# Performance work log

Hardware: AMD Instinct MI355X
Metric: run time of the kernel (lower is better)

## Reference

```python
import jax, jax.numpy as jnp
import numpy as np

B, S, HID = 2, 2048, 2048
H, KVH, D = 32, 4, 128
EPS = 1e-6
ROPE_THETA = 1e6
INIT = 0.02


def setup_inputs() -> dict:
    key = jax.random.key(0)
    ks = jax.random.split(key, 6)
    hidden_states = jax.random.normal(ks[0], (B, S, HID), jnp.float32)
    q_w = jax.random.normal(ks[1], (HID, H * D), jnp.float32) * INIT
    k_w = jax.random.normal(ks[2], (HID, KVH * D), jnp.float32) * INIT
    v_w = jax.random.normal(ks[3], (HID, KVH * D), jnp.float32) * INIT
    o_w = jax.random.normal(ks[4], (H * D, HID), jnp.float32) * INIT
    q_norm_w = jnp.ones((D,), jnp.float32)
    k_norm_w = jnp.ones((D,), jnp.float32)
    # rotary embeddings, computed once per position (B, S, D)
    pos = jnp.arange(S, dtype=jnp.float32)
    inv_freq = 1.0 / (ROPE_THETA ** (jnp.arange(0, D, 2, dtype=jnp.float32) / D))
    freqs = pos[:, None] * inv_freq[None, :]          # (S, D/2)
    emb = jnp.concatenate([freqs, freqs], axis=-1)    # (S, D)
    cos = jnp.broadcast_to(jnp.cos(emb)[None], (B, S, D))
    sin = jnp.broadcast_to(jnp.sin(emb)[None], (B, S, D))
    # causal mask (is_causal=True, sliding_window=None)
    attn_mask = jnp.tril(jnp.ones((S, S), bool))[None, None]  # (1,1,S,S)
    return {"hidden_states": hidden_states, "cos": cos, "sin": sin,
            "q_w": q_w, "k_w": k_w, "v_w": v_w, "o_w": o_w,
            "q_norm_w": q_norm_w, "k_norm_w": k_norm_w, "attn_mask": attn_mask}


def _rms_norm(x, w):
    xf = x.astype(jnp.float32)
    var = jnp.mean(jax.lax.square(xf), axis=-1, keepdims=True)
    return (w * (xf * jax.lax.rsqrt(var + EPS))).astype(x.dtype)


def _rotate_half(x):
    x1, x2 = jnp.split(x, 2, axis=-1)
    return jnp.concatenate([-x2, x1], axis=-1)


def _apply_rope(q, k, cos, sin):
    # q: (B,H,S,D), k: (B,KVH,S,D); cos/sin: (B,S,D) -> (B,1,S,D)
    cos = cos[:, None]
    sin = sin[:, None]
    q = q * cos + _rotate_half(q) * sin
    k = k * cos + _rotate_half(k) * sin
    return q, k


def reference(hidden_states, cos, sin, q_w, k_w, v_w, o_w, q_norm_w, k_norm_w, attn_mask):
    b, s, _ = hidden_states.shape
    scaling = D ** (-0.5)
    # projections + per-head QK RMSNorm
    q = _rms_norm((hidden_states @ q_w).reshape(b, s, H, D), q_norm_w)
    k = _rms_norm((hidden_states @ k_w).reshape(b, s, KVH, D), k_norm_w)
    v = (hidden_states @ v_w).reshape(b, s, KVH, D)
    q = jnp.transpose(q, (0, 2, 1, 3))   # (b,H,s,D)
    k = jnp.transpose(k, (0, 2, 1, 3))   # (b,KVH,s,D)
    v = jnp.transpose(v, (0, 2, 1, 3))
    q, k = _apply_rope(q, k, cos, sin)
    # GQA: repeat KV heads across groups
    groups = H // KVH
    k = jnp.repeat(k, groups, axis=1)    # (b,H,s,D)
    v = jnp.repeat(v, groups, axis=1)
    # eager softmax attention (fp32 softmax)
    scores = jnp.einsum('bhqd,bhkd->bhqk', q, k).astype(jnp.float32) * scaling
    scores = jnp.where(attn_mask, scores, jnp.float32(-1e30))
    probs = jax.nn.softmax(scores, axis=-1).astype(q.dtype)
    attn = jnp.einsum('bhqk,bhkd->bhqd', probs, v)
    attn = jnp.transpose(attn, (0, 2, 1, 3)).reshape(b, s, H * D)
    return attn @ o_w
```

## Files before the change

kernel.cpp:

```cpp
#include <hip/hip_runtime.h>
#include <hip/hip_bf16.h>

typedef unsigned short u16;
typedef __attribute__((ext_vector_type(4))) float f32x4;
typedef __attribute__((ext_vector_type(16))) float f32x16;
typedef __attribute__((ext_vector_type(8))) short bf16x8;
typedef __attribute__((ext_vector_type(4))) unsigned u32x4;

#define B_ 2
#define S_ 2048
#define HID_ 2048
#define H_ 32
#define KVH_ 4
#define D_ 128
#define M_ 4096
#define NQ_ 4096
#define NKV_ 512

typedef const __attribute__((address_space(1))) void gconst_void;
typedef __attribute__((address_space(3))) void lds_void;

static __device__ __forceinline__ void gload_lds16(const void* g, void* l) {
  __builtin_amdgcn_global_load_lds((gconst_void*)g, (lds_void*)l, 16, 0, 0);
}

#define WAITV(N) asm volatile("s_waitcnt vmcnt(" #N ")" ::: "memory")
#define WAITL0() asm volatile("s_waitcnt lgkmcnt(0)" ::: "memory")

static __device__ __forceinline__ u16 f2b(float f) {
  union { float f; unsigned i; } x; x.f = f;
  return (u16)((x.i + 0x7fffu + ((x.i >> 16) & 1u)) >> 16);
}
static __device__ __forceinline__ float b2f(u16 u) {
  union { unsigned i; float f; } x; x.i = ((unsigned)u) << 16;
  return x.f;
}

__global__ void k_cvt(const float* __restrict__ in, u16* __restrict__ out, int n4) {
  int i = blockIdx.x * blockDim.x + threadIdx.x;
  int stride = gridDim.x * blockDim.x;
  for (; i < n4; i += stride) {
    float4 v = reinterpret_cast<const float4*>(in)[i];
    ushort4 o;
    o.x = f2b(v.x); o.y = f2b(v.y); o.z = f2b(v.z); o.w = f2b(v.w);
    reinterpret_cast<ushort4*>(out)[i] = o;
  }
}

__global__ __launch_bounds__(256) void k_transpose(const float* __restrict__ W,
                                                   u16* __restrict__ Wt, int K, int N) {
  __shared__ u16 t[64][72];
  int n0 = blockIdx.x * 64, k0 = blockIdx.y * 64;
  int tid = threadIdx.x;
  int r = tid >> 4;
  int c4 = (tid & 15) * 4;
#pragma unroll
  for (int i = 0; i < 4; i++) {
    int k = r + i * 16;
    float4 v = *reinterpret_cast<const float4*>(W + (size_t)(k0 + k) * N + n0 + c4);
    t[k][c4 + 0] = f2b(v.x); t[k][c4 + 1] = f2b(v.y);
    t[k][c4 + 2] = f2b(v.z); t[k][c4 + 3] = f2b(v.w);
  }
  __syncthreads();
#pragma unroll
  for (int i = 0; i < 4; i++) {
    int n = r + i * 16;
    ushort4 o;
    o.x = t[c4 + 0][n]; o.y = t[c4 + 1][n]; o.z = t[c4 + 2][n]; o.w = t[c4 + 3][n];
    *reinterpret_cast<ushort4*>(Wt + (size_t)(n0 + n) * K + k0 + c4) = o;
  }
}

__device__ __forceinline__ void gemm_core(const u16* __restrict__ A, const u16* __restrict__ Bt,
                                          int K, int m0, int n0,
                                          u16* As, u16* Bs, f32x4 (&acc)[4][4]) {
  const int tid = threadIdx.x;
  const int lane = tid & 63;
  const int wid = tid >> 6;
  const int wr = wid >> 1, wc = wid & 1;
  const int lrow = lane & 15;
  const int hi = lane >> 4;
  const f32x4 zz = {0.f, 0.f, 0.f, 0.f};
#pragma unroll
  for (int i = 0; i < 4; i++)
#pragma unroll
    for (int j = 0; j < 4; j++) acc[i][j] = zz;

  const int srow = tid >> 3;
  const int sc16 = tid & 7;
  const int nk = K >> 6;
  int cur = 0;

#pragma unroll
  for (int rep = 0; rep < 4; rep++) {
    int row = rep * 32 + srow;
    int gcol = ((sc16 ^ (row & 7)) << 3);
    gload_lds16(A + (size_t)(m0 + row) * K + gcol, As + row * 64 + sc16 * 8);
    gload_lds16(Bt + (size_t)(n0 + row) * K + gcol, Bs + row * 64 + sc16 * 8);
  }
  __syncthreads();

  for (int t = 0; t < nk; t++) {
    if (t + 1 < nk) {
      int nxt = cur ^ 1;
      int kb = (t + 1) << 6;
#pragma unroll
      for (int rep = 0; rep < 4; rep++) {
        int row = rep * 32 + srow;
        int gcol = kb + ((sc16 ^ (row & 7)) << 3);
        gload_lds16(A + (size_t)(m0 + row) * K + gcol, As + nxt * 8192 + row * 64 + sc16 * 8);
        gload_lds16(Bt + (size_t)(n0 + row) * K + gcol, Bs + nxt * 8192 + row * 64 + sc16 * 8);
      }
    }
    const u16* Ac = As + cur * 8192;
    const u16* Bc = Bs + cur * 8192;
#pragma unroll
    for (int kc = 0; kc < 2; kc++) {
      bf16x8 af[4], bfr[4];
#pragma unroll
      for (int i = 0; i < 4; i++) {
        int row = wr * 64 + i * 16 + lrow;
        af[i] = *reinterpret_cast<const bf16x8*>(Ac + row * 64 + ((((kc << 2) + hi) ^ (row & 7)) << 3));
      }
#pragma unroll
      for (int j = 0; j < 4; j++) {
        int row = wc * 64 + j * 16 + lrow;
        bfr[j] = *reinterpret_cast<const bf16x8*>(Bc + row * 64 + ((((kc << 2) + hi) ^ (row & 7)) << 3));
      }
#pragma unroll
      for (int i = 0; i < 4; i++)
#pragma unroll
        for (int j = 0; j < 4; j++)
          acc[i][j] = __builtin_amdgcn_mfma_f32_16x16x32_bf16(af[i], bfr[j], acc[i][j], 0, 0, 0);
    }
    __syncthreads();
    cur ^= 1;
  }
}

__global__ __launch_bounds__(512, 2) void k_gemm_q8(const u16* __restrict__ A,
    const u16* __restrict__ Bt, u16* __restrict__ qb) {
  __shared__ u16 Ash[2][2][128 * 64];
  __shared__ u16 Bsh[2][2][128 * 64];
  const int bid = blockIdx.x;
  const int wg = (bid & 7) * 32 + (bid >> 3);
  const int mt = wg & 15, nt = wg >> 4;
  const int m0 = mt * 256, n0 = nt * 256;
  const int K = HID_, nk = K >> 6;
  const int tid = threadIdx.x, lane = tid & 63;
  const int wv = tid >> 6, wr = wv >> 2, wc = wv & 3;
  const int lrow = lane & 15, hi4 = lane >> 4;

  const int s0r = tid >> 3, sc = tid & 7;
  const int s1r = (tid + 512) >> 3;

  auto stgA = [&](int h, int t, int d) {
    gload_lds16(A + (size_t)(m0 + h * 128 + s0r) * K + t * 64 + ((sc ^ (s0r & 7)) << 3),
                &Ash[d][h][s0r * 64 + sc * 8]);
    gload_lds16(A + (size_t)(m0 + h * 128 + s1r) * K + t * 64 + ((sc ^ (s1r & 7)) << 3),
                &Ash[d][h][s1r * 64 + sc * 8]);
  };
  auto stgB = [&](int h, int t, int d) {
    gload_lds16(Bt + (size_t)(n0 + h * 128 + s0r) * K + t * 64 + ((sc ^ (s0r & 7)) << 3),
                &Bsh[d][h][s0r * 64 + sc * 8]);
    gload_lds16(Bt + (size_t)(n0 + h * 128 + s1r) * K + t * 64 + ((sc ^ (s1r & 7)) << 3),
                &Bsh[d][h][s1r * 64 + sc * 8]);
  };

  f32x4 acc[8][4];
  const f32x4 zz = {0.f, 0.f, 0.f, 0.f};
#pragma unroll
  for (int f = 0; f < 8; f++)
#pragma unroll
    for (int j = 0; j < 4; j++) acc[f][j] = zz;

  bf16x8 af[4][2], bfr[2][2];

  auto lda = [&](int mh, int d) {
#pragma unroll
    for (int fi = 0; fi < 4; fi++) {
      int row = fi * 32 + wr * 16 + lrow;
#pragma unroll
      for (int kk = 0; kk < 2; kk++)
        af[fi][kk] = *reinterpret_cast<const bf16x8*>(
            &Ash[d][mh][row * 64 + ((((kk << 2) + hi4) ^ (row & 7)) << 3)]);
    }
  };
  auto ldb = [&](int nh, int d) {
#pragma unroll
    for (int ji = 0; ji < 2; ji++) {
      int row = ji * 64 + wc * 16 + lrow;
#pragma unroll
      for (int kk = 0; kk < 2; kk++)
        bfr[ji][kk] = *reinterpret_cast<const bf16x8*>(
            &Bsh[d][nh][row * 64 + ((((kk << 2) + hi4) ^ (row & 7)) << 3)]);
    }
  };
  auto mq = [&](int mh, int nh) {
    __builtin_amdgcn_s_setprio(1);
#pragma unroll
    for (int kk = 0; kk < 2; kk++)
#pragma unroll
      for (int fi = 0; fi < 4; fi++)
#pragma unroll
        for (int ji = 0; ji < 2; ji++)
          acc[mh * 4 + fi][nh * 2 + ji] = __builtin_amdgcn_mfma_f32_16x16x32_bf16(
              af[fi][kk], bfr[ji][kk], acc[mh * 4 + fi][nh * 2 + ji], 0, 0, 0);
    __builtin_amdgcn_s_setprio(0);
  };

  stgA(0, 0, 0); stgB(0, 0, 0); stgA(1, 0, 0); stgB(1, 0, 0);
  WAITV(0);
  __builtin_amdgcn_s_barrier();

  for (int t = 0; t < nk; t++) {
    const int d = t & 1, nd = d ^ 1;
    const bool pre = (t + 1 < nk);
    if (pre) { stgA(0, t + 1, nd); stgB(0, t + 1, nd); }
    lda(0, d); ldb(0, d);
    WAITV(6);
    __builtin_amdgcn_sched_barrier(0);
    __builtin_amdgcn_s_barrier();
    WAITL0();
    __builtin_amdgcn_sched_barrier(0);
    mq(0, 0);
    __builtin_amdgcn_s_barrier();
    if (pre) stgA(1, t + 1, nd);
    lda(1, d);
    WAITV(6);
    __builtin_amdgcn_sched_barrier(0);
    __builtin_amdgcn_s_barrier();
    WAITL0();
    __builtin_amdgcn_sched_barrier(0);
    mq(1, 0);
    __builtin_amdgcn_s_barrier();
    if (pre) stgB(1, t + 1, nd);
    ldb(1, d);
    __builtin_amdgcn_sched_barrier(0);
    __builtin_amdgcn_s_barrier();
    WAITL0();
    __builtin_amdgcn_sched_barrier(0);
    mq(1, 1);
    __builtin_amdgcn_s_barrier();
    lda(0, d);
    WAITV(4);
    __builtin_amdgcn_sched_barrier(0);
    __builtin_amdgcn_s_barrier();
    WAITL0();
    __builtin_amdgcn_sched_barrier(0);
    mq(0, 1);
    __builtin_amdgcn_s_barrier();
  }

  const int lr4 = hi4 * 4, lc = lane & 15;
#pragma unroll
  for (int f = 0; f < 8; f++)
#pragma unroll
    for (int j = 0; j < 4; j++)
#pragma unroll
      for (int rr = 0; rr < 4; rr++) {
        int m = m0 + f * 32 + wr * 16 + lr4 + rr;
        int ncol = n0 + j * 64 + wc * 16 + lc;
        int b = m >> 11, s = m & (S_ - 1);
        int head = ncol >> 7, dd = ncol & 127;
        qb[(((size_t)b * H_ + head) * S_ + s) * D_ + dd] = f2b(acc[f][j][rr]);
      }
}

__global__ __launch_bounds__(256, 2) void k_gemm_kv(const u16* __restrict__ hb,
    const u16* __restrict__ kwt, const u16* __restrict__ vwt,
    u16* __restrict__ kb, u16* __restrict__ vb) {
  __shared__ u16 As[2 * 128 * 64], Bs[2 * 128 * 64];
  const int bid = blockIdx.x;
  const int wg = (bid & 7) * 32 + (bid >> 3);
  const int mt = wg & 31, nt = wg >> 5;
  const bool isv = nt >= 4;
  const int head = isv ? nt - 4 : nt;
  const u16* Bt = isv ? vwt : kwt;
  f32x4 acc[4][4];
  gemm_core(hb, Bt, HID_, mt * 128, head * 128, As, Bs, acc);
  const int lane = threadIdx.x & 63;
  const int wid = threadIdx.x >> 6;
  const int wr = wid >> 1, wc = wid & 1;
  const int lr4 = (lane >> 4) * 4, lc = lane & 15;
#pragma unroll
  for (int i = 0; i < 4; i++)
#pragma unroll
    for (int j = 0; j < 4; j++)
#pragma unroll
      for (int r = 0; r < 4; r++) {
        int m = mt * 128 + wr * 64 + i * 16 + lr4 + r;
        int d = wc * 64 + j * 16 + lc;
        int b = m >> 11, s = m & (S_ - 1);
        u16 val = f2b(acc[i][j][r]);
        if (isv) vb[(((size_t)b * KVH_ + head) * D_ + d) * S_ + s] = val;
        else     kb[(((size_t)b * KVH_ + head) * S_ + s) * D_ + d] = val;
      }
}

__global__ __launch_bounds__(256, 2) void k_gemm_o(const u16* __restrict__ ab,
    const u16* __restrict__ owt, float* __restrict__ out) {
  __shared__ u16 As[2 * 128 * 64], Bs[2 * 128 * 64];
  const int bid = blockIdx.x;
  const int wg = (bid & 7) * 64 + (bid >> 3);
  const int mt = wg & 31, nt = wg >> 5;
  f32x4 acc[4][4];
  gemm_core(ab, owt, NQ_, mt * 128, nt * 128, As, Bs, acc);
  const int lane = threadIdx.x & 63;
  const int wid = threadIdx.x >> 6;
  const int wr = wid >> 1, wc = wid & 1;
  const int lr4 = (lane >> 4) * 4, lc = lane & 15;
#pragma unroll
  for (int i = 0; i < 4; i++)
#pragma unroll
    for (int j = 0; j < 4; j++)
#pragma unroll
      for (int r = 0; r < 4; r++) {
        int m = mt * 128 + wr * 64 + i * 16 + lr4 + r;
        int n = nt * 128 + wc * 64 + j * 16 + lc;
        out[(size_t)m * HID_ + n] = acc[i][j][r];
      }
}

__global__ __launch_bounds__(256) void k_norm_rope(u16* __restrict__ qb, u16* __restrict__ kb,
    const float* __restrict__ cosp, const float* __restrict__ sinp,
    const float* __restrict__ qnw, const float* __restrict__ knw) {
  int row = blockIdx.x * 4 + (threadIdx.x >> 6);
  int lane = threadIdx.x & 63;
  const int QROWS = B_ * H_ * S_;
  u16* ptr; const float* nw; int b, s;
  if (row < QROWS) {
    ptr = qb + (size_t)row * D_; nw = qnw;
    s = row & (S_ - 1); b = row / (H_ * S_);
  } else {
    int r2 = row - QROWS;
    ptr = kb + (size_t)r2 * D_; nw = knw;
    s = r2 & (S_ - 1); b = r2 / (KVH_ * S_);
  }
  int d = lane * 2;
  float x0 = b2f(ptr[d]), x1 = b2f(ptr[d + 1]);
  float ss = x0 * x0 + x1 * x1;
#pragma unroll
  for (int m = 1; m < 64; m <<= 1) ss += __shfl_xor(ss, m);
  float inv = rsqrtf(ss * (1.0f / 128.0f) + 1e-6f);
  x0 = x0 * inv * nw[d]; x1 = x1 * inv * nw[d + 1];
  float p0 = __shfl_xor(x0, 32), p1 = __shfl_xor(x1, 32);
  float r0 = (lane < 32) ? -p0 : p0;
  float r1 = (lane < 32) ? -p1 : p1;
  const float* cp = cosp + ((size_t)b * S_ + s) * D_;
  const float* sp = sinp + ((size_t)b * S_ + s) * D_;
  ptr[d]     = f2b(x0 * cp[d]     + r0 * sp[d]);
  ptr[d + 1] = f2b(x1 * cp[d + 1] + r1 * sp[d + 1]);
}

__global__ __launch_bounds__(512, 2) void k_attn(const u16* __restrict__ q,
    const u16* __restrict__ k, const u16* __restrict__ vt, u16* __restrict__ out) {
  __shared__ u16 Kb[2 * 64 * 128];
  __shared__ u16 Vb[2 * 128 * 64];
  const int bid = blockIdx.x;
  const int wg = (bid & 7) * 32 + (bid >> 3);
  const int qx = wg & 3, bh = wg >> 2;
  const int b = bh >> 5, h = bh & 31;
  const int kvh = h >> 3;
  const int tid = threadIdx.x, lane = tid & 63, w = tid >> 6;
  const int lq = lane & 31, hi = lane >> 5;
  const u16* qp  = q  + ((size_t)(b * H_ + h) * S_) * D_;
  const u16* kp  = k  + ((size_t)(b * KVH_ + kvh) * S_) * D_;
  const u16* vtp = vt + ((size_t)(b * KVH_ + kvh) * D_) * S_;

  const int rowKa = tid >> 4;
  const int colK  = ((tid & 15) ^ (rowKa & 15)) << 3;
  const int rowVa = tid >> 3;
  const int colV  = ((tid & 7) ^ (rowVa & 7)) << 3;

  const float KSC = 0.08838834764831845f * 1.44269504088896340f;
  const f32x16 z16 = {0.f};

  int cur = 0;
  for (int half = 0; half < 2; half++) {
    const int qt = half ? (7 - qx) : qx;
    const int q0 = qt * 256;
    const int last = 4 * qt + 3;
    const int qg = q0 + 32 * w + lq;

    {
      u16* kd = Kb + cur * 8192 + tid * 8;
      u16* vd = Vb + cur * 8192 + tid * 8;
      gload_lds16(kp + (size_t)rowKa * D_ + colK, kd);
      gload_lds16(kp + (size_t)(rowKa + 32) * D_ + colK, kd + 4096);
      gload_lds16(vtp + (size_t)rowVa * S_ + colV, vd);
      gload_lds16(vtp + (size_t)(rowVa + 64) * S_ + colV, vd + 4096);
    }

    bf16x8 qf[8];
#pragma unroll
    for (int ds = 0; ds < 8; ds++)
      qf[ds] = *reinterpret_cast<const bf16x8*>(qp + (size_t)qg * D_ + ds * 16 + hi * 8);

    f32x16 oacc[4];
#pragma unroll
    for (int dt = 0; dt < 4; dt++) oacc[dt] = z16;
    float mrun = -1e30f, lrun = 0.f;

    __syncthreads();

    for (int nt = 0; nt <= last; nt++) {
      const int n0 = nt * 64;
      if (nt < last) {
        const int n1 = n0 + 64;
        u16* kd = Kb + (cur ^ 1) * 8192 + tid * 8;
        u16* vd = Vb + (cur ^ 1) * 8192 + tid * 8;
        gload_lds16(kp + (size_t)(n1 + rowKa) * D_ + colK, kd);
        gload_lds16(kp + (size_t)(n1 + rowKa + 32) * D_ + colK, kd + 4096);
        gload_lds16(vtp + (size_t)rowVa * S_ + n1 + colV, vd);
        gload_lds16(vtp + (size_t)(rowVa + 64) * S_ + n1 + colV, vd + 4096);
      }
      const u16* Kc = Kb + cur * 8192;
      const u16* Vc = Vb + cur * 8192;

      const bool skip = (n0 > q0 + 32 * w + 31);
      if (!skip) {
        const bool needmask = (n0 + 63 > q0 + 32 * w);

        f32x16 sacc[2];
        sacc[0] = z16; sacc[1] = z16;
#pragma unroll
        for (int ds = 0; ds < 8; ds++) {
          const int sl = (((ds << 1) + hi) ^ (lq & 15)) << 3;
          bf16x8 ka0 = *reinterpret_cast<const bf16x8*>(Kc + lq * 128 + sl);
          bf16x8 ka1 = *reinterpret_cast<const bf16x8*>(Kc + (lq + 32) * 128 + sl);
          __builtin_amdgcn_s_setprio(1);
          sacc[0] = __builtin_amdgcn_mfma_f32_32x32x16_bf16(ka0, qf[ds], sacc[0], 0, 0, 0);
          sacc[1] = __builtin_amdgcn_mfma_f32_32x32x16_bf16(ka1, qf[ds], sacc[1], 0, 0, 0);
          __builtin_amdgcn_s_setprio(0);
        }

        float tm = -1e30f;
#pragma unroll
        for (int t = 0; t < 2; t++)
#pragma unroll
          for (int r = 0; r < 16; r++) {
            float s2 = sacc[t][r] * KSC;
            if (needmask) {
              int kvg = n0 + 32 * t + (r & 3) + 8 * (r >> 2) + 4 * hi;
              if (kvg > qg) s2 = -1e30f;
            }
            sacc[t][r] = s2;
            tm = fmaxf(tm, s2);
          }
        tm = fmaxf(tm, __shfl_xor(tm, 32));
        if (__any(tm > mrun + 8.f)) {
          float mn = fmaxf(mrun, tm);
          float al = exp2f(mrun - mn);
          mrun = mn;
          lrun *= al;
#pragma unroll
          for (int r = 0; r < 16; r++) {
            float ar = __shfl(al, (r & 3) + 8 * (r >> 2) + 4 * hi);
#pragma unroll
            for (int dt = 0; dt < 4; dt++) oacc[dt][r] *= ar;
          }
        }
        float rs = 0.f;
#pragma unroll
        for (int t = 0; t < 2; t++)
#pragma unroll
          for (int r = 0; r < 16; r++) {
            float pv = exp2f(sacc[t][r] - mrun);
            sacc[t][r] = pv;
            rs += pv;
          }
        rs += __shfl_xor(rs, 32);
        lrun += rs;

        u32x4 pa[4];
#pragma unroll
        for (int t = 0; t < 2; t++)
#pragma unroll
          for (int ksl = 0; ksl < 2; ksl++) {
            unsigned wa, wb, wc2, wd;
            asm("v_cvt_pk_bf16_f32 %0, %1, %2" : "=v"(wa)
                : "v"(sacc[t][8 * ksl + 0]), "v"(sacc[t][8 * ksl + 1]));
            asm("v_cvt_pk_bf16_f32 %0, %1, %2" : "=v"(wb)
                : "v"(sacc[t][8 * ksl + 2]), "v"(sacc[t][8 * ksl + 3]));
            asm("v_cvt_pk_bf16_f32 %0, %1, %2" : "=v"(wc2)
                : "v"(sacc[t][8 * ksl + 4]), "v"(sacc[t][8 * ksl + 5]));
            asm("v_cvt_pk_bf16_f32 %0, %1, %2" : "=v"(wd)
                : "v"(sacc[t][8 * ksl + 6]), "v"(sacc[t][8 * ksl + 7]));
            asm("v_permlane32_swap_b32 %0, %1" : "+v"(wa), "+v"(wc2));
            asm("v_permlane32_swap_b32 %0, %1" : "+v"(wb), "+v"(wd));
            u32x4 t4 = {wa, wb, wc2, wd};
            pa[t * 2 + ksl] = t4;
          }

#pragma unroll
        for (int ks = 0; ks < 4; ks++) {
          bf16x8 paf = __builtin_bit_cast(bf16x8, pa[ks]);
          bf16x8 bv[4];
#pragma unroll
          for (int dt = 0; dt < 4; dt++) {
            int rowv = dt * 32 + lq;
            bv[dt] = *reinterpret_cast<const bf16x8*>(
                Vc + rowv * 64 + ((((ks << 1) + hi) ^ (rowv & 7)) << 3));
          }
          __builtin_amdgcn_s_setprio(1);
#pragma unroll
          for (int dt = 0; dt < 4; dt++)
            oacc[dt] = __builtin_amdgcn_mfma_f32_32x32x16_bf16(paf, bv[dt], oacc[dt], 0, 0, 0);
          __builtin_amdgcn_s_setprio(0);
        }
      }
      __syncthreads();
      cur ^= 1;
    }

    float linv = 1.0f / lrun;
#pragma unroll
    for (int r = 0; r < 16; r++) {
      const int idx_r = (r & 3) + 8 * (r >> 2) + 4 * hi;
      float lr = __shfl(linv, idx_r);
      size_t base = ((size_t)b * S_ + (q0 + 32 * w + idx_r)) * NQ_ + h * D_ + lq;
#pragma unroll
      for (int dt = 0; dt < 4; dt++)
        out[base + dt * 32] = f2b(oacc[dt][r] * lr);
    }
  }
}

extern "C" void kernel_launch(void* const* d_in, const int* in_sizes, int n_in,
                              void* d_out, int out_size, void* d_ws, size_t ws_size,
                              hipStream_t stream) {
  const float* hidden = (const float*)d_in[0];
  const float* cosp   = (const float*)d_in[1];
  const float* sinp   = (const float*)d_in[2];
  const float* q_w    = (const float*)d_in[3];
  const float* k_w    = (const float*)d_in[4];
  const float* v_w    = (const float*)d_in[5];
  const float* o_w    = (const float*)d_in[6];
  const float* qnw    = (const float*)d_in[7];
  const float* knw    = (const float*)d_in[8];

  char* p = (char*)d_ws;
  u16* hb  = (u16*)p; p += (size_t)M_ * HID_ * 2;
  u16* qwt = (u16*)p; p += (size_t)NQ_ * HID_ * 2;
  u16* kwt = (u16*)p; p += (size_t)NKV_ * HID_ * 2;
  u16* vwt = (u16*)p; p += (size_t)NKV_ * HID_ * 2;
  u16* owt = (u16*)p; p += (size_t)HID_ * NQ_ * 2;
  u16* qb  = (u16*)p; p += (size_t)B_ * H_ * S_ * D_ * 2;
  u16* kb  = (u16*)p; p += (size_t)B_ * KVH_ * S_ * D_ * 2;
  u16* vb  = (u16*)p; p += (size_t)B_ * KVH_ * S_ * D_ * 2;
  u16* ab  = (u16*)p; p += (size_t)M_ * NQ_ * 2;

  k_cvt<<<2048, 256, 0, stream>>>(hidden, hb, M_ * HID_ / 4);
  k_transpose<<<dim3(NQ_ / 64, HID_ / 64), 256, 0, stream>>>(q_w, qwt, HID_, NQ_);
  k_transpose<<<dim3(NKV_ / 64, HID_ / 64), 256, 0, stream>>>(k_w, kwt, HID_, NKV_);
  k_transpose<<<dim3(NKV_ / 64, HID_ / 64), 256, 0, stream>>>(v_w, vwt, HID_, NKV_);
  k_transpose<<<dim3(HID_ / 64, NQ_ / 64), 256, 0, stream>>>(o_w, owt, NQ_, HID_);
  k_gemm_q8<<<256, 512, 0, stream>>>(hb, qwt, qb);
  k_gemm_kv<<<256, 256, 0, stream>>>(hb, kwt, vwt, kb, vb);
  k_norm_rope<<<(B_ * H_ * S_ + B_ * KVH_ * S_) / 4, 256, 0, stream>>>(qb, kb, cosp, sinp, qnw, knw);
  k_attn<<<256, 512, 0, stream>>>(qb, kb, vb, ab);
  k_gemm_o<<<512, 256, 0, stream>>>(ab, owt, (float*)d_out);
}
```

Baseline: 361.2 us.

## Fuse prep kernels, fold softmax scale into norm, split attention grid, repipeline Q GEMM

```diff
diff --git a/kernel.cpp b/kernel.cpp
--- a/kernel.cpp
+++ b/kernel.cpp
@@ -26,6 +26,8 @@
 
 #define WAITV(N) asm volatile("s_waitcnt vmcnt(" #N ")" ::: "memory")
 #define WAITL0() asm volatile("s_waitcnt lgkmcnt(0)" ::: "memory")
+#define SBAR() __builtin_amdgcn_s_barrier()
+#define SCHED0() __builtin_amdgcn_sched_barrier(0)
 
 static __device__ __forceinline__ u16 f2b(float f) {
   union { float f; unsigned i; } x; x.f = f;
@@ -35,22 +37,14 @@
   union { unsigned i; float f; } x; x.i = ((unsigned)u) << 16;
   return x.f;
 }
-
-__global__ void k_cvt(const float* __restrict__ in, u16* __restrict__ out, int n4) {
-  int i = blockIdx.x * blockDim.x + threadIdx.x;
-  int stride = gridDim.x * blockDim.x;
-  for (; i < n4; i += stride) {
-    float4 v = reinterpret_cast<const float4*>(in)[i];
-    ushort4 o;
-    o.x = f2b(v.x); o.y = f2b(v.y); o.z = f2b(v.z); o.w = f2b(v.w);
-    reinterpret_cast<ushort4*>(out)[i] = o;
-  }
-}
-
-__global__ __launch_bounds__(256) void k_transpose(const float* __restrict__ W,
-                                                   u16* __restrict__ Wt, int K, int N) {
-  __shared__ u16 t[64][72];
-  int n0 = blockIdx.x * 64, k0 = blockIdx.y * 64;
+static __device__ __forceinline__ float max3f(float a, float b, float c) {
+  float d;
+  asm("v_max3_f32 %0, %1, %2, %3" : "=v"(d) : "v"(a), "v"(b), "v"(c));
+  return d;
+}
+
+static __device__ __forceinline__ void tr_tile(const float* __restrict__ W,
+    u16* __restrict__ Wt, int K, int N, int n0, int k0, u16 (*t)[72]) {
   int tid = threadIdx.x;
   int r = tid >> 4;
   int c4 = (tid & 15) * 4;
@@ -68,6 +62,38 @@
     ushort4 o;
     o.x = t[c4 + 0][n]; o.y = t[c4 + 1][n]; o.z = t[c4 + 2][n]; o.w = t[c4 + 3][n];
     *reinterpret_cast<ushort4*>(Wt + (size_t)(n0 + n) * K + k0 + c4) = o;
+  }
+}
+
+__global__ __launch_bounds__(256) void k_prep(const float* __restrict__ hidden, u16* __restrict__ hb,
+    const float* __restrict__ qw, u16* __restrict__ qwt,
+    const float* __restrict__ kw, u16* __restrict__ kwt,
+    const float* __restrict__ vw, u16* __restrict__ vwt,
+    const float* __restrict__ ow, u16* __restrict__ owt) {
+  __shared__ u16 t[64][72];
+  const int bid = blockIdx.x;
+  if (bid < 2048) {
+    const int n4 = M_ * HID_ / 4;
+    int i = bid * 256 + threadIdx.x;
+    const int stride = 2048 * 256;
+    for (; i < n4; i += stride) {
+      float4 v = reinterpret_cast<const float4*>(hidden)[i];
+      ushort4 o;
+      o.x = f2b(v.x); o.y = f2b(v.y); o.z = f2b(v.z); o.w = f2b(v.w);
+      reinterpret_cast<ushort4*>(hb)[i] = o;
+    }
+  } else if (bid < 4096) {
+    int l = bid - 2048;
+    tr_tile(qw, qwt, HID_, NQ_, (l & 63) * 64, (l >> 6) * 64, t);
+  } else if (bid < 4352) {
+    int l = bid - 4096;
+    tr_tile(kw, kwt, HID_, NKV_, (l & 7) * 64, (l >> 3) * 64, t);
+  } else if (bid < 4608) {
+    int l = bid - 4352;
+    tr_tile(vw, vwt, HID_, NKV_, (l & 7) * 64, (l >> 3) * 64, t);
+  } else {
+    int l = bid - 4608;
+    tr_tile(ow, owt, NQ_, HID_, (l & 31) * 64, (l >> 5) * 64, t);
   }
 }
 
@@ -174,15 +200,15 @@
 #pragma unroll
     for (int j = 0; j < 4; j++) acc[f][j] = zz;
 
-  bf16x8 af[4][2], bfr[2][2];
-
-  auto lda = [&](int mh, int d) {
+  bf16x8 af0[4][2], af1[4][2], bfr[2][2];
+
+  auto lda = [&](bf16x8 (&dst)[4][2], int mh, int d) {
 #pragma unroll
     for (int fi = 0; fi < 4; fi++) {
       int row = fi * 32 + wr * 16 + lrow;
 #pragma unroll
       for (int kk = 0; kk < 2; kk++)
-        af[fi][kk] = *reinterpret_cast<const bf16x8*>(
+        dst[fi][kk] = *reinterpret_cast<const bf16x8*>(
             &Ash[d][mh][row * 64 + ((((kk << 2) + hi4) ^ (row & 7)) << 3)]);
     }
   };
@@ -196,7 +222,7 @@
             &Bsh[d][nh][row * 64 + ((((kk << 2) + hi4) ^ (row & 7)) << 3)]);
     }
   };
-  auto mq = [&](int mh, int nh) {
+  auto mq = [&](bf16x8 (&afh)[4][2], int mh, int nh) {
     __builtin_amdgcn_s_setprio(1);
 #pragma unroll
     for (int kk = 0; kk < 2; kk++)
@@ -205,51 +231,39 @@
 #pragma unroll
         for (int ji = 0; ji < 2; ji++)
           acc[mh * 4 + fi][nh * 2 + ji] = __builtin_amdgcn_mfma_f32_16x16x32_bf16(
-              af[fi][kk], bfr[ji][kk], acc[mh * 4 + fi][nh * 2 + ji], 0, 0, 0);
+              afh[fi][kk], bfr[ji][kk], acc[mh * 4 + fi][nh * 2 + ji], 0, 0, 0);
     __builtin_amdgcn_s_setprio(0);
   };
 
-  stgA(0, 0, 0); stgB(0, 0, 0); stgA(1, 0, 0); stgB(1, 0, 0);
-  WAITV(0);
-  __builtin_amdgcn_s_barrier();
+  stgA(0, 0, 0); stgA(1, 0, 0); stgB(0, 0, 0); stgB(1, 0, 0);
+  WAITV(2); SCHED0();
+  SBAR(); SCHED0();
 
   for (int t = 0; t < nk; t++) {
     const int d = t & 1, nd = d ^ 1;
     const bool pre = (t + 1 < nk);
-    if (pre) { stgA(0, t + 1, nd); stgB(0, t + 1, nd); }
-    lda(0, d); ldb(0, d);
-    WAITV(6);
-    __builtin_amdgcn_sched_barrier(0);
-    __builtin_amdgcn_s_barrier();
-    WAITL0();
-    __builtin_amdgcn_sched_barrier(0);
-    mq(0, 0);
-    __builtin_amdgcn_s_barrier();
+    lda(af0, 0, d); ldb(0, d);
+    if (pre) stgA(0, t + 1, nd);
+    SCHED0(); SBAR();
+    WAITL0(); SCHED0();
+    mq(af0, 0, 0);
+    SBAR(); SCHED0();
+    lda(af1, 1, d);
     if (pre) stgA(1, t + 1, nd);
-    lda(1, d);
-    WAITV(6);
-    __builtin_amdgcn_sched_barrier(0);
-    __builtin_amdgcn_s_barrier();
-    WAITL0();
-    __builtin_amdgcn_sched_barrier(0);
-    mq(1, 0);
-    __builtin_amdgcn_s_barrier();
+    WAITV(4); SCHED0(); SBAR();
+    WAITL0(); SCHED0();
+    mq(af1, 1, 0);
+    SBAR(); SCHED0();
+    ldb(1, d);
+    if (pre) stgB(0, t + 1, nd);
+    SCHED0(); SBAR();
+    WAITL0(); SCHED0();
+    mq(af1, 1, 1);
+    SBAR(); SCHED0();
     if (pre) stgB(1, t + 1, nd);
-    ldb(1, d);
-    __builtin_amdgcn_sched_barrier(0);
-    __builtin_amdgcn_s_barrier();
-    WAITL0();
-    __builtin_amdgcn_sched_barrier(0);
-    mq(1, 1);
-    __builtin_amdgcn_s_barrier();
-    lda(0, d);
-    WAITV(4);
-    __builtin_amdgcn_sched_barrier(0);
-    __builtin_amdgcn_s_barrier();
-    WAITL0();
-    __builtin_amdgcn_sched_barrier(0);
-    mq(0, 1);
-    __builtin_amdgcn_s_barrier();
+    WAITV(2); SCHED0(); SBAR();
+    mq(af0, 0, 1);
+    SBAR(); SCHED0();
   }
 
   const int lr4 = hi4 * 4, lc = lane & 15;
@@ -328,21 +342,23 @@
   int row = blockIdx.x * 4 + (threadIdx.x >> 6);
   int lane = threadIdx.x & 63;
   const int QROWS = B_ * H_ * S_;
-  u16* ptr; const float* nw; int b, s;
+  u16* ptr; const float* nw; int b, s; float os;
   if (row < QROWS) {
     ptr = qb + (size_t)row * D_; nw = qnw;
     s = row & (S_ - 1); b = row / (H_ * S_);
+    os = 0.08838834764831845f * 1.44269504088896340f;
   } else {
     int r2 = row - QROWS;
     ptr = kb + (size_t)r2 * D_; nw = knw;
     s = r2 & (S_ - 1); b = r2 / (KVH_ * S_);
+    os = 1.0f;
   }
   int d = lane * 2;
   float x0 = b2f(ptr[d]), x1 = b2f(ptr[d + 1]);
   float ss = x0 * x0 + x1 * x1;
 #pragma unroll
   for (int m = 1; m < 64; m <<= 1) ss += __shfl_xor(ss, m);
-  float inv = rsqrtf(ss * (1.0f / 128.0f) + 1e-6f);
+  float inv = rsqrtf(ss * (1.0f / 128.0f) + 1e-6f) * os;
   x0 = x0 * inv * nw[d]; x1 = x1 * inv * nw[d + 1];
   float p0 = __shfl_xor(x0, 32), p1 = __shfl_xor(x1, 32);
   float r0 = (lane < 32) ? -p0 : p0;
@@ -353,13 +369,13 @@
   ptr[d + 1] = f2b(x1 * cp[d + 1] + r1 * sp[d + 1]);
 }
 
-__global__ __launch_bounds__(512, 2) void k_attn(const u16* __restrict__ q,
+__global__ __launch_bounds__(512, 4) void k_attn(const u16* __restrict__ q,
     const u16* __restrict__ k, const u16* __restrict__ vt, u16* __restrict__ out) {
   __shared__ u16 Kb[2 * 64 * 128];
   __shared__ u16 Vb[2 * 128 * 64];
   const int bid = blockIdx.x;
-  const int wg = (bid & 7) * 32 + (bid >> 3);
-  const int qx = wg & 3, bh = wg >> 2;
+  const int qt = (bid < 256) ? (7 - (bid >> 6)) : ((bid - 256) >> 6);
+  const int bh = bid & 63;
   const int b = bh >> 5, h = bh & 31;
   const int kvh = h >> 3;
   const int tid = threadIdx.x, lane = tid & 63, w = tid >> 6;
@@ -373,157 +389,154 @@
   const int rowVa = tid >> 3;
   const int colV  = ((tid & 7) ^ (rowVa & 7)) << 3;
 
-  const float KSC = 0.08838834764831845f * 1.44269504088896340f;
   const f32x16 z16 = {0.f};
+  const int q0 = qt * 256;
+  const int last = 4 * qt + 3;
+  const int qg = q0 + 32 * w + lq;
+
+  {
+    u16* kd = Kb + tid * 8;
+    u16* vd = Vb + tid * 8;
+    gload_lds16(kp + (size_t)rowKa * D_ + colK, kd);
+    gload_lds16(kp + (size_t)(rowKa + 32) * D_ + colK, kd + 4096);
+    gload_lds16(vtp + (size_t)rowVa * S_ + colV, vd);
+    gload_lds16(vtp + (size_t)(rowVa + 64) * S_ + colV, vd + 4096);
+  }
+
+  bf16x8 qf[8];
+#pragma unroll
+  for (int ds = 0; ds < 8; ds++)
+    qf[ds] = *reinterpret_cast<const bf16x8*>(qp + (size_t)qg * D_ + ds * 16 + hi * 8);
+
+  f32x16 oacc[4];
+#pragma unroll
+  for (int dt = 0; dt < 4; dt++) oacc[dt] = z16;
+  float mrun = -1e30f, lrun = 0.f;
+
+  __syncthreads();
 
   int cur = 0;
-  for (int half = 0; half < 2; half++) {
-    const int qt = half ? (7 - qx) : qx;
-    const int q0 = qt * 256;
-    const int last = 4 * qt + 3;
-    const int qg = q0 + 32 * w + lq;
-
-    {
-      u16* kd = Kb + cur * 8192 + tid * 8;
-      u16* vd = Vb + cur * 8192 + tid * 8;
-      gload_lds16(kp + (size_t)rowKa * D_ + colK, kd);
-      gload_lds16(kp + (size_t)(rowKa + 32) * D_ + colK, kd + 4096);
-      gload_lds16(vtp + (size_t)rowVa * S_ + colV, vd);
-      gload_lds16(vtp + (size_t)(rowVa + 64) * S_ + colV, vd + 4096);
-    }
-
-    bf16x8 qf[8];
-#pragma unroll
-    for (int ds = 0; ds < 8; ds++)
-      qf[ds] = *reinterpret_cast<const bf16x8*>(qp + (size_t)qg * D_ + ds * 16 + hi * 8);
-
-    f32x16 oacc[4];
-#pragma unroll
-    for (int dt = 0; dt < 4; dt++) oacc[dt] = z16;
-    float mrun = -1e30f, lrun = 0.f;
-
+  for (int nt = 0; nt <= last; nt++) {
+    const int n0 = nt * 64;
+    if (nt < last) {
+      const int n1 = n0 + 64;
+      u16* kd = Kb + (cur ^ 1) * 8192 + tid * 8;
+      u16* vd = Vb + (cur ^ 1) * 8192 + tid * 8;
+      gload_lds16(kp + (size_t)(n1 + rowKa) * D_ + colK, kd);
+      gload_lds16(kp + (size_t)(n1 + rowKa + 32) * D_ + colK, kd + 4096);
+      gload_lds16(vtp + (size_t)rowVa * S_ + n1 + colV, vd);
+      gload_lds16(vtp + (size_t)(rowVa + 64) * S_ + n1 + colV, vd + 4096);
+    }
+    const u16* Kc = Kb + cur * 8192;
+    const u16* Vc = Vb + cur * 8192;
+
+    const bool skip = (n0 > q0 + 32 * w + 31);
+    if (!skip) {
+      const bool needmask = (n0 + 63 > q0 + 32 * w);
+
+      f32x16 sacc[2];
+      sacc[0] = z16; sacc[1] = z16;
+#pragma unroll
+      for (int ds = 0; ds < 8; ds++) {
+        const int sl = (((ds << 1) + hi) ^ (lq & 15)) << 3;
+        bf16x8 ka0 = *reinterpret_cast<const bf16x8*>(Kc + lq * 128 + sl);
+        bf16x8 ka1 = *reinterpret_cast<const bf16x8*>(Kc + (lq + 32) * 128 + sl);
+        __builtin_amdgcn_s_setprio(1);
+        sacc[0] = __builtin_amdgcn_mfma_f32_32x32x16_bf16(ka0, qf[ds], sacc[0], 0, 0, 0);
+        sacc[1] = __builtin_amdgcn_mfma_f32_32x32x16_bf16(ka1, qf[ds], sacc[1], 0, 0, 0);
+        __builtin_amdgcn_s_setprio(0);
+      }
+
+      if (needmask) {
+#pragma unroll
+        for (int t = 0; t < 2; t++)
+#pragma unroll
+          for (int r = 0; r < 16; r++) {
+            int kvg = n0 + 32 * t + (r & 3) + 8 * (r >> 2) + 4 * hi;
+            if (kvg > qg) sacc[t][r] = -1e30f;
+          }
+      }
+      float tm = fmaxf(sacc[0][0], sacc[0][1]);
+#pragma unroll
+      for (int i = 1; i < 16; i++) {
+        const int e0 = 2 * i, e1 = 2 * i + 1;
+        tm = max3f(tm, sacc[e0 >> 4][e0 & 15], sacc[e1 >> 4][e1 & 15]);
+      }
+      tm = fmaxf(tm, __shfl_xor(tm, 32));
+      if (__any(tm > mrun + 8.f)) {
+        float mn = fmaxf(mrun, tm);
+        float al = exp2f(mrun - mn);
+        mrun = mn;
+        lrun *= al;
+#pragma unroll
+        for (int r = 0; r < 16; r++) {
+          float ar = __shfl(al, (r & 3) + 8 * (r >> 2) + 4 * hi);
+#pragma unroll
+          for (int dt = 0; dt < 4; dt++) oacc[dt][r] *= ar;
+        }
+      }
+      float rs = 0.f;
+#pragma unroll
+      for (int t = 0; t < 2; t++)
+#pragma unroll
+        for (int r = 0; r < 16; r++) {
+          float pv = exp2f(sacc[t][r] - mrun);
+          sacc[t][r] = pv;
+          rs += pv;
+        }
+      rs += __shfl_xor(rs, 32);
+      lrun += rs;
+
+      u32x4 pa[4];
+#pragma unroll
+      for (int t = 0; t < 2; t++)
+#pragma unroll
+        for (int ksl = 0; ksl < 2; ksl++) {
+          unsigned wa, wb, wc2, wd;
+          asm("v_cvt_pk_bf16_f32 %0, %1, %2" : "=v"(wa)
+              : "v"(sacc[t][8 * ksl + 0]), "v"(sacc[t][8 * ksl + 1]));
+          asm("v_cvt_pk_bf16_f32 %0, %1, %2" : "=v"(wb)
+              : "v"(sacc[t][8 * ksl + 2]), "v"(sacc[t][8 * ksl + 3]));
+          asm("v_cvt_pk_bf16_f32 %0, %1, %2" : "=v"(wc2)
+              : "v"(sacc[t][8 * ksl + 4]), "v"(sacc[t][8 * ksl + 5]));
+          asm("v_cvt_pk_bf16_f32 %0, %1, %2" : "=v"(wd)
+              : "v"(sacc[t][8 * ksl + 6]), "v"(sacc[t][8 * ksl + 7]));
+          asm("v_permlane32_swap_b32 %0, %1" : "+v"(wa), "+v"(wc2));
+          asm("v_permlane32_swap_b32 %0, %1" : "+v"(wb), "+v"(wd));
+          u32x4 t4 = {wa, wb, wc2, wd};
+          pa[t * 2 + ksl] = t4;
+        }
+
+#pragma unroll
+      for (int ks = 0; ks < 4; ks++) {
+        bf16x8 paf = __builtin_bit_cast(bf16x8, pa[ks]);
+        bf16x8 bv[4];
+#pragma unroll
+        for (int dt = 0; dt < 4; dt++) {
+          int rowv = dt * 32 + lq;
+          bv[dt] = *reinterpret_cast<const bf16x8*>(
+              Vc + rowv * 64 + ((((ks << 1) + hi) ^ (rowv & 7)) << 3));
+        }
+        __builtin_amdgcn_s_setprio(1);
+#pragma unroll
+        for (int dt = 0; dt < 4; dt++)
+          oacc[dt] = __builtin_amdgcn_mfma_f32_32x32x16_bf16(paf, bv[dt], oacc[dt], 0, 0, 0);
+        __builtin_amdgcn_s_setprio(0);
+      }
+    }
     __syncthreads();
-
-    for (int nt = 0; nt <= last; nt++) {
-      const int n0 = nt * 64;
-      if (nt < last) {
-        const int n1 = n0 + 64;
-        u16* kd = Kb + (cur ^ 1) * 8192 + tid * 8;
-        u16* vd = Vb + (cur ^ 1) * 8192 + tid * 8;
-        gload_lds16(kp + (size_t)(n1 + rowKa) * D_ + colK, kd);
-        gload_lds16(kp + (size_t)(n1 + rowKa + 32) * D_ + colK, kd + 4096);
-        gload_lds16(vtp + (size_t)rowVa * S_ + n1 + colV, vd);
-        gload_lds16(vtp + (size_t)(rowVa + 64) * S_ + n1 + colV, vd + 4096);
-      }
-      const u16* Kc = Kb + cur * 8192;
-      const u16* Vc = Vb + cur * 8192;
-
-      const bool skip = (n0 > q0 + 32 * w + 31);
-      if (!skip) {
-        const bool needmask = (n0 + 63 > q0 + 32 * w);
-
-        f32x16 sacc[2];
-        sacc[0] = z16; sacc[1] = z16;
-#pragma unroll
-        for (int ds = 0; ds < 8; ds++) {
-          const int sl = (((ds << 1) + hi) ^ (lq & 15)) << 3;
-          bf16x8 ka0 = *reinterpret_cast<const bf16x8*>(Kc + lq * 128 + sl);
-          bf16x8 ka1 = *reinterpret_cast<const bf16x8*>(Kc + (lq + 32) * 128 + sl);
-          __builtin_amdgcn_s_setprio(1);
-          sacc[0] = __builtin_amdgcn_mfma_f32_32x32x16_bf16(ka0, qf[ds], sacc[0], 0, 0, 0);
-          sacc[1] = __builtin_amdgcn_mfma_f32_32x32x16_bf16(ka1, qf[ds], sacc[1], 0, 0, 0);
-          __builtin_amdgcn_s_setprio(0);
-        }
-
-        float tm = -1e30f;
-#pragma unroll
-        for (int t = 0; t < 2; t++)
-#pragma unroll
-          for (int r = 0; r < 16; r++) {
-            float s2 = sacc[t][r] * KSC;
-            if (needmask) {
-              int kvg = n0 + 32 * t + (r & 3) + 8 * (r >> 2) + 4 * hi;
-              if (kvg > qg) s2 = -1e30f;
-            }
-            sacc[t][r] = s2;
-            tm = fmaxf(tm, s2);
-          }
-        tm = fmaxf(tm, __shfl_xor(tm, 32));
-        if (__any(tm > mrun + 8.f)) {
-          float mn = fmaxf(mrun, tm);
-          float al = exp2f(mrun - mn);
-          mrun = mn;
-          lrun *= al;
-#pragma unroll
-          for (int r = 0; r < 16; r++) {
-            float ar = __shfl(al, (r & 3) + 8 * (r >> 2) + 4 * hi);
-#pragma unroll
-            for (int dt = 0; dt < 4; dt++) oacc[dt][r] *= ar;
-          }
-        }
-        float rs = 0.f;
-#pragma unroll
-        for (int t = 0; t < 2; t++)
-#pragma unroll
-          for (int r = 0; r < 16; r++) {
-            float pv = exp2f(sacc[t][r] - mrun);
-            sacc[t][r] = pv;
-            rs += pv;
-          }
-        rs += __shfl_xor(rs, 32);
-        lrun += rs;
-
-        u32x4 pa[4];
-#pragma unroll
-        for (int t = 0; t < 2; t++)
-#pragma unroll
-          for (int ksl = 0; ksl < 2; ksl++) {
-            unsigned wa, wb, wc2, wd;
-            asm("v_cvt_pk_bf16_f32 %0, %1, %2" : "=v"(wa)
-                : "v"(sacc[t][8 * ksl + 0]), "v"(sacc[t][8 * ksl + 1]));
-            asm("v_cvt_pk_bf16_f32 %0, %1, %2" : "=v"(wb)
-                : "v"(sacc[t][8 * ksl + 2]), "v"(sacc[t][8 * ksl + 3]));
-            asm("v_cvt_pk_bf16_f32 %0, %1, %2" : "=v"(wc2)
-                : "v"(sacc[t][8 * ksl + 4]), "v"(sacc[t][8 * ksl + 5]));
-            asm("v_cvt_pk_bf16_f32 %0, %1, %2" : "=v"(wd)
-                : "v"(sacc[t][8 * ksl + 6]), "v"(sacc[t][8 * ksl + 7]));
-            asm("v_permlane32_swap_b32 %0, %1" : "+v"(wa), "+v"(wc2));
-            asm("v_permlane32_swap_b32 %0, %1" : "+v"(wb), "+v"(wd));
-            u32x4 t4 = {wa, wb, wc2, wd};
-            pa[t * 2 + ksl] = t4;
-          }
-
-#pragma unroll
-        for (int ks = 0; ks < 4; ks++) {
-          bf16x8 paf = __builtin_bit_cast(bf16x8, pa[ks]);
-          bf16x8 bv[4];
-#pragma unroll
-          for (int dt = 0; dt < 4; dt++) {
-            int rowv = dt * 32 + lq;
-            bv[dt] = *reinterpret_cast<const bf16x8*>(
-                Vc + rowv * 64 + ((((ks << 1) + hi) ^ (rowv & 7)) << 3));
-          }
-          __builtin_amdgcn_s_setprio(1);
-#pragma unroll
-          for (int dt = 0; dt < 4; dt++)
-            oacc[dt] = __builtin_amdgcn_mfma_f32_32x32x16_bf16(paf, bv[dt], oacc[dt], 0, 0, 0);
-          __builtin_amdgcn_s_setprio(0);
-        }
-      }
-      __syncthreads();
-      cur ^= 1;
-    }
-
-    float linv = 1.0f / lrun;
-#pragma unroll
-    for (int r = 0; r < 16; r++) {
-      const int idx_r = (r & 3) + 8 * (r >> 2) + 4 * hi;
-      float lr = __shfl(linv, idx_r);
-      size_t base = ((size_t)b * S_ + (q0 + 32 * w + idx_r)) * NQ_ + h * D_ + lq;
-#pragma unroll
-      for (int dt = 0; dt < 4; dt++)
-        out[base + dt * 32] = f2b(oacc[dt][r] * lr);
-    }
+    cur ^= 1;
+  }
+
+  float linv = 1.0f / lrun;
+#pragma unroll
+  for (int r = 0; r < 16; r++) {
+    const int idx_r = (r & 3) + 8 * (r >> 2) + 4 * hi;
+    float lr = __shfl(linv, idx_r);
+    size_t base = ((size_t)b * S_ + (q0 + 32 * w + idx_r)) * NQ_ + h * D_ + lq;
+#pragma unroll
+    for (int dt = 0; dt < 4; dt++)
+      out[base + dt * 32] = f2b(oacc[dt][r] * lr);
   }
 }
 
@@ -551,14 +564,10 @@
   u16* vb  = (u16*)p; p += (size_t)B_ * KVH_ * S_ * D_ * 2;
   u16* ab  = (u16*)p; p += (size_t)M_ * NQ_ * 2;
 
-  k_cvt<<<2048, 256, 0, stream>>>(hidden, hb, M_ * HID_ / 4);
-  k_transpose<<<dim3(NQ_ / 64, HID_ / 64), 256, 0, stream>>>(q_w, qwt, HID_, NQ_);
-  k_transpose<<<dim3(NKV_ / 64, HID_ / 64), 256, 0, stream>>>(k_w, kwt, HID_, NKV_);
-  k_transpose<<<dim3(NKV_ / 64, HID_ / 64), 256, 0, stream>>>(v_w, vwt, HID_, NKV_);
-  k_transpose<<<dim3(HID_ / 64, NQ_ / 64), 256, 0, stream>>>(o_w, owt, NQ_, HID_);
+  k_prep<<<6656, 256, 0, stream>>>(hidden, hb, q_w, qwt, k_w, kwt, v_w, vwt, o_w, owt);
   k_gemm_q8<<<256, 512, 0, stream>>>(hb, qwt, qb);
   k_gemm_kv<<<256, 256, 0, stream>>>(hb, kwt, vwt, kb, vb);
   k_norm_rope<<<(B_ * H_ * S_ + B_ * KVH_ * S_) / 4, 256, 0, stream>>>(qb, kb, cosp, sinp, qnw, knw);
-  k_attn<<<256, 512, 0, stream>>>(qb, kb, vb, ab);
+  k_attn<<<512, 512, 0, stream>>>(qb, kb, vb, ab);
   k_gemm_o<<<512, 256, 0, stream>>>(ab, owt, (float*)d_out);
 }
```

After: 546.3 us. 51.3% more time.
